# Kernel tuning notes

Hardware: AMD Instinct MI355X
Metric: run time of the kernel (lower is better)

The kernel has to match this reference:

```python
import jax, jax.numpy as jnp
import numpy as np

N = 100000
E = 1600000
IN_DIM, HID, OUT = 128, 64, 32
SLOPE = 0.1


def setup_inputs() -> dict:
    key = jax.random.key(0)
    ks = jax.random.split(key, 8)
    x = jax.random.normal(ks[0], (N, IN_DIM), dtype=jnp.float32)
    edge_index = jax.random.randint(ks[1], (2, E), 0, N, dtype=jnp.int64)
    s1 = 1.0 / np.sqrt(IN_DIM)
    s2 = 1.0 / np.sqrt(HID)
    W_l1 = jax.random.uniform(ks[2], (IN_DIM, HID), jnp.float32, -s1, s1)
    W_r1 = jax.random.uniform(ks[3], (IN_DIM, HID), jnp.float32, -s1, s1)
    b1 = jax.random.uniform(ks[4], (HID,), jnp.float32, -s1, s1)
    W_l2 = jax.random.uniform(ks[5], (HID, OUT), jnp.float32, -s2, s2)
    W_r2 = jax.random.uniform(ks[6], (HID, OUT), jnp.float32, -s2, s2)
    b2 = jax.random.uniform(ks[7], (OUT,), jnp.float32, -s2, s2)
    return {"x": x, "edge_index": edge_index,
            "W_l1": W_l1, "W_r1": W_r1, "b1": b1,
            "W_l2": W_l2, "W_r2": W_r2, "b2": b2}


def _sage_conv(h, src, dst, deg_inv, W_l, W_r, b):
    # mean-aggregate neighbor features: gather from src, scatter-add to dst
    agg = jax.ops.segment_sum(h[src], dst, num_segments=N) * deg_inv  # [N, d]
    return agg @ W_l + h @ W_r + b


def reference(x, edge_index, W_l1, W_r1, b1, W_l2, W_r2, b2):
    src, dst = edge_index[0], edge_index[1]
    deg = jax.ops.segment_sum(jnp.ones((E,), x.dtype), dst, num_segments=N)
    deg_inv = (1.0 / jnp.maximum(deg, 1.0))[:, None]  # [N, 1]
    h = jax.nn.leaky_relu(_sage_conv(x, src, dst, deg_inv, W_l1, W_r1, b1), SLOPE)
    z = jax.nn.leaky_relu(_sage_conv(h, src, dst, deg_inv, W_l2, W_r2, b2), SLOPE)
    return z
```

## Files before the change

kernel.cpp:

```cpp
#include <hip/hip_runtime.h>


constexpr int IN_DIM  = 128;
constexpr int HID     = 64;
constexpr int OUT_DIM = 32;
constexpr float SLOPE = 0.1f;
constexpr int NPB_SHIFT = 8;
constexpr int NBMAX = 512;
constexpr int CHUNK = 4096;
constexpr int SUBCAP = 4096;

typedef unsigned int uint32;
typedef unsigned short ushort16;
typedef unsigned char uchar8;
using floatx2 = __attribute__((ext_vector_type(2))) float;

__device__ inline float blo(uint32 u) { return __uint_as_float(u << 16); }
__device__ inline float bhi(uint32 u) { return __uint_as_float(u & 0xffff0000u); }
__device__ inline ushort16 f2b(float f) {
    uint32 u = __float_as_uint(f);
    u += 0x7fffu + ((u >> 16) & 1u);
    return (ushort16)(u >> 16);
}
__device__ inline uint32 pack2(float lo, float hi) {
    return (uint32)f2b(lo) | ((uint32)f2b(hi) << 16);
}
__device__ inline float lrelu(float v) { return (v > 0.f) ? v : SLOPE * v; }
__device__ inline void addup(float* acc, uint4 u) {
    acc[0] += blo(u.x); acc[1] += bhi(u.x);
    acc[2] += blo(u.y); acc[3] += bhi(u.y);
    acc[4] += blo(u.z); acc[5] += bhi(u.z);
    acc[6] += blo(u.w); acc[7] += bhi(u.w);
}
__device__ inline uchar8 f2fp8(float f) {
    uint32 r = (uint32)__builtin_amdgcn_cvt_pk_fp8_f32(f, f, 0, false);
    return (uchar8)(r & 0xffu);
}
__device__ inline void addp4(float* acc, uint32 w) {
    floatx2 a = __builtin_amdgcn_cvt_pk_f32_fp8((int)w, false);
    floatx2 b = __builtin_amdgcn_cvt_pk_f32_fp8((int)w, true);
    acc[0] += a[0]; acc[1] += a[1]; acc[2] += b[0]; acc[3] += b[1];
}
__device__ inline void addq(float* acc, uint4 u) {
    addp4(acc + 0, u.x); addp4(acc + 4, u.y);
    addp4(acc + 8, u.z); addp4(acc + 12, u.w);
}

__global__ __launch_bounds__(256) void prep_kernel(
    const float* __restrict__ Wl1, const float* __restrict__ Wr1,
    const float* __restrict__ Wl2, const float* __restrict__ Wr2,
    ushort16* __restrict__ Wb1, ushort16* __restrict__ Wb2,
    int* __restrict__ bhist, int* __restrict__ done) {
    const int gid = blockIdx.x * 256 + threadIdx.x;
    if (gid < NBMAX) bhist[gid] = 0;
    if (gid == NBMAX) *done = 0;
    for (int i = gid; i < 128 * 128; i += gridDim.x * 256) {
        int c = i >> 7, k = i & 127;
        Wb1[i] = f2b((c < HID) ? Wl1[k * HID + c] : Wr1[k * HID + (c - HID)]);
    }
    for (int i = gid; i < 64 * 64; i += gridDim.x * 256) {
        int c = i >> 6, k = i & 63;
        Wb2[i] = f2b((c < OUT_DIM) ? Wl2[k * OUT_DIM + c]
                                   : Wr2[k * OUT_DIM + (c - OUT_DIM)]);
    }
}

__global__ __launch_bounds__(256) void hist_scan_kernel(
    const int* __restrict__ dst, int* __restrict__ bhist,
    int* __restrict__ pbase, int* __restrict__ bcur,
    int* __restrict__ done, int E, int NB) {
    __shared__ int bh[NBMAX];
    __shared__ int s2[256];
    __shared__ int flag;
    const int tid = threadIdx.x;
    for (int i = tid; i < NBMAX; i += 256) bh[i] = 0;
    __syncthreads();
    for (int e = blockIdx.x * 256 + tid; e < E; e += gridDim.x * 256)
        atomicAdd(&bh[dst[e] >> NPB_SHIFT], 1);
    __syncthreads();
    for (int b = tid; b < NBMAX; b += 256)
        if (bh[b]) atomicAdd(&bhist[b], bh[b]);
    __threadfence();
    if (tid == 0) flag = (atomicAdd(done, 1) == (int)gridDim.x - 1) ? 1 : 0;
    __syncthreads();
    if (!flag) return;
    __threadfence();
    int v0 = atomicAdd(&bhist[2 * tid], 0);
    int v1 = atomicAdd(&bhist[2 * tid + 1], 0);
    int p0 = (v0 + 15) & ~15, p1 = (v1 + 15) & ~15;
    s2[tid] = p0 + p1; __syncthreads();
    for (int off = 1; off < 256; off <<= 1) {
        int b = (tid >= off) ? s2[tid - off] : 0;
        __syncthreads();
        s2[tid] += b;
        __syncthreads();
    }
    int base = s2[tid] - (p0 + p1);
    pbase[2 * tid]     = base;      bcur[2 * tid]     = base;
    pbase[2 * tid + 1] = base + p0; bcur[2 * tid + 1] = base + p0;
}

__global__ __launch_bounds__(256) void gemm1_part_kernel(
    const float* __restrict__ x, const ushort16* __restrict__ Wb1,
    const float* __restrict__ b1,
    const int* __restrict__ src, const int* __restrict__ dst,
    int* __restrict__ bcur, uint32* __restrict__ pairs,
    uchar8* __restrict__ xlb, float* __restrict__ xr,
    int N, int E, int NB, int npart) {
    using frag = __attribute__((ext_vector_type(8))) short;
    using f32x4 = __attribute__((ext_vector_type(4))) float;
    constexpr int LDA = IN_DIM + 8;
    __shared__ union {
        struct {
            int hist[NBMAX], loff[NBMAX], cur[NBMAX], gbase[NBMAX];
            int s[256];
            uint32 stage[CHUNK];
        } p;
        ushort16 Ash[64][LDA];
    } sm;
    const int tid = threadIdx.x;
    if (blockIdx.x < npart) {
        const int e0  = blockIdx.x * CHUNK;
        const int cnt = min(CHUNK, E - e0);
        for (int i = tid; i < NBMAX; i += 256) sm.p.hist[i] = 0;
        __syncthreads();
        int sreg[16], dreg[16];
#pragma unroll
        for (int k = 0; k < 16; ++k) {
            int i = tid + k * 256;
            if (i < cnt) {
                sreg[k] = src[e0 + i];
                dreg[k] = dst[e0 + i];
                atomicAdd(&sm.p.hist[dreg[k] >> NPB_SHIFT], 1);
            }
        }
        __syncthreads();
        int a0 = sm.p.hist[2 * tid], a1 = sm.p.hist[2 * tid + 1];
        sm.p.s[tid] = a0 + a1; __syncthreads();
        for (int off = 1; off < 256; off <<= 1) {
            int t = (tid >= off) ? sm.p.s[tid - off] : 0;
            __syncthreads();
            sm.p.s[tid] += t;
            __syncthreads();
        }
        int ex = sm.p.s[tid] - (a0 + a1);
        sm.p.loff[2 * tid] = ex;      sm.p.loff[2 * tid + 1] = ex + a0;
        sm.p.cur[2 * tid]  = ex;      sm.p.cur[2 * tid + 1]  = ex + a0;
        __syncthreads();
#pragma unroll
        for (int k = 0; k < 16; ++k) {
            int i = tid + k * 256;
            if (i < cnt) {
                int b = dreg[k] >> NPB_SHIFT;
                int pos = atomicAdd(&sm.p.cur[b], 1);
                sm.p.stage[pos] = (uint32)sreg[k] | ((uint32)(dreg[k] & 255) << 24);
            }
        }
        __syncthreads();
        for (int b = tid; b < NB; b += 256) {
            int cb = sm.p.hist[b];
            if (cb) sm.p.gbase[b] = atomicAdd(&bcur[b], cb);
        }
        __syncthreads();
        for (int i = tid; i < cnt; i += 256) {
            int lo = 0, hi = NB - 1;
            while (lo < hi) {
                int mid = (lo + hi + 1) >> 1;
                if (sm.p.loff[mid] <= i) lo = mid; else hi = mid - 1;
            }
            pairs[sm.p.gbase[lo] + (i - sm.p.loff[lo])] = sm.p.stage[i];
        }
        return;
    }
    const int n0 = (blockIdx.x - npart) * 64;
    {
        const int lc = (tid & 31) * 4;
        for (int row = tid >> 5; row < 64; row += 8) {
            int node = n0 + row;
            float4 xv = (node < N)
                ? *reinterpret_cast<const float4*>(&x[(long)node * IN_DIM + lc])
                : float4{0.f, 0.f, 0.f, 0.f};
            ushort16 pk[4] = {f2b(xv.x), f2b(xv.y), f2b(xv.z), f2b(xv.w)};
            *reinterpret_cast<ushort2*>(&sm.Ash[row][lc])     = ushort2{pk[0], pk[1]};
            *reinterpret_cast<ushort2*>(&sm.Ash[row][lc + 2]) = ushort2{pk[2], pk[3]};
        }
    }
    __syncthreads();
    const int lane = tid & 63;
    const int m0   = (tid >> 6) * 16;
    const int mlo  = lane & 15;
    const int qk   = lane >> 4;
    frag Af[4];
#pragma unroll
    for (int kc = 0; kc < 4; ++kc)
        Af[kc] = *reinterpret_cast<const frag*>(&sm.Ash[m0 + mlo][kc * 32 + qk * 8]);
#pragma unroll
    for (int ct = 0; ct < 8; ++ct) {
        f32x4 acc = {0.f, 0.f, 0.f, 0.f};
#pragma unroll
        for (int kc = 0; kc < 4; ++kc) {
            frag Bf = *reinterpret_cast<const frag*>(
                &Wb1[(ct * 16 + mlo) * 128 + kc * 32 + qk * 8]);
            acc = __builtin_amdgcn_mfma_f32_16x16x32_bf16(Af[kc], Bf, acc, 0, 0, 0);
        }
        const int col = ct * 16 + mlo;
#pragma unroll
        for (int r = 0; r < 4; ++r) {
            int node = n0 + m0 + qk * 4 + r;
            if (node < N) {
                if (col < HID) xlb[(long)node * HID + col] = f2fp8(acc[r]);
                else           xr[(long)node * HID + (col - HID)] = acc[r] + b1[col - HID];
            }
        }
    }
}

__global__ __launch_bounds__(512) void agg1_gemm2_kernel(
    const uint32* __restrict__ pairs, const int* __restrict__ bhist,
    const int* __restrict__ pbase,
    const uint4* __restrict__ xlq, const float* __restrict__ xr,
    const ushort16* __restrict__ Wb2, const float* __restrict__ b2,
    uint32* __restrict__ srcs, int* __restrict__ rowptr, int* __restrict__ degA,
    ushort16* __restrict__ hl, float* __restrict__ hr, int N) {
    using frag = __attribute__((ext_vector_type(8))) short;
    using f32x4 = __attribute__((ext_vector_type(4))) float;
    constexpr int LDH = HID + 8;
    __shared__ int hist[256], loff[256], cur[128];
    __shared__ int lsrc[SUBCAP];
    __shared__ ushort16 hsh[128][LDH];
    const int tid  = threadIdx.x;
    const int bkt  = blockIdx.x >> 1;
    const int half = blockIdx.x & 1;
    const int n0   = bkt << NPB_SHIFT;
    const int base = pbase[bkt];
    const int sz   = bhist[bkt];
    if (tid < 256) hist[tid] = 0;
    __syncthreads();
    for (int i = tid; i < sz; i += 512)
        atomicAdd(&hist[pairs[base + i] >> 24], 1);
    __syncthreads();
    int v = (tid < 256) ? hist[tid] : 0;
    if (tid < 256) loff[tid] = v;
    __syncthreads();
    for (int off = 1; off < 256; off <<= 1) {
        int t = (tid >= off && tid < 256) ? loff[tid - off] : 0;
        __syncthreads();
        if (tid < 256) loff[tid] += t;
        __syncthreads();
    }
    if (tid < 256) loff[tid] -= v;
    __syncthreads();
    if (half == 0 && tid < 256 && n0 + tid < N) {
        rowptr[n0 + tid] = base + loff[tid];
        degA[n0 + tid]   = hist[tid];
    }
    const int hbase = loff[half << 7];
    const int hcnt  = (half ? sz : loff[128]) - hbase;
    if (tid < 128) cur[tid] = loff[(half << 7) + tid] - hbase;
    __syncthreads();
    for (int i = tid; i < sz; i += 512) {
        uint32 u = pairs[base + i];
        int dl = u >> 24;
        if ((dl >> 7) == half) {
            int pos = atomicAdd(&cur[dl & 127], 1);
            lsrc[pos] = (int)(u & 0xFFFFFFu);
        }
    }
    __syncthreads();
    for (int i = tid; i < hcnt; i += 512)
        srcs[base + hbase + i] = (uint32)lsrc[i];
    const int lane = tid & 63;
    const int wid  = tid >> 6;
    const int li   = lane & 3;
    {
        const int nlb = wid * 16 + (lane >> 2);
        const int nl  = (half << 7) + nlb;
        const int n   = n0 + nl;
        if (n < N) {
            const int lo0 = loff[nl] - hbase;
            const int d   = hist[nl];
            float acc[16] = {};
            int j = 0;
            while (j + 16 <= d) {
                int i0[8], i1[8];
#pragma unroll
                for (int t = 0; t < 8; ++t) i0[t] = lsrc[lo0 + j + t];
#pragma unroll
                for (int t = 0; t < 8; ++t) i1[t] = lsrc[lo0 + j + 8 + t];
                uint4 u0[8], u1[8];
#pragma unroll
                for (int t = 0; t < 8; ++t) u0[t] = xlq[(long)i0[t] * 4 + li];
#pragma unroll
                for (int t = 0; t < 8; ++t) u1[t] = xlq[(long)i1[t] * 4 + li];
#pragma unroll
                for (int t = 0; t < 8; ++t) { addq(acc, u0[t]); addq(acc, u1[t]); }
                j += 16;
            }
            if (j + 8 <= d) {
                int i0[8];
#pragma unroll
                for (int t = 0; t < 8; ++t) i0[t] = lsrc[lo0 + j + t];
                uint4 u0[8];
#pragma unroll
                for (int t = 0; t < 8; ++t) u0[t] = xlq[(long)i0[t] * 4 + li];
#pragma unroll
                for (int t = 0; t < 8; ++t) addq(acc, u0[t]);
                j += 8;
            }
            for (; j < d; ++j) {
                uint4 u = xlq[(long)lsrc[lo0 + j] * 4 + li];
                addq(acc, u);
            }
            const float dinv = (d > 0) ? (1.f / (float)d) : 1.f;
            const float* xrp = &xr[(long)n * HID + li * 16];
            float4 xa = *reinterpret_cast<const float4*>(xrp);
            float4 xb = *reinterpret_cast<const float4*>(xrp + 4);
            float4 xc = *reinterpret_cast<const float4*>(xrp + 8);
            float4 xd = *reinterpret_cast<const float4*>(xrp + 12);
            float hv[16];
            hv[0]  = fmaf(acc[0],  dinv, xa.x); hv[1]  = fmaf(acc[1],  dinv, xa.y);
            hv[2]  = fmaf(acc[2],  dinv, xa.z); hv[3]  = fmaf(acc[3],  dinv, xa.w);
            hv[4]  = fmaf(acc[4],  dinv, xb.x); hv[5]  = fmaf(acc[5],  dinv, xb.y);
            hv[6]  = fmaf(acc[6],  dinv, xb.z); hv[7]  = fmaf(acc[7],  dinv, xb.w);
            hv[8]  = fmaf(acc[8],  dinv, xc.x); hv[9]  = fmaf(acc[9],  dinv, xc.y);
            hv[10] = fmaf(acc[10], dinv, xc.z); hv[11] = fmaf(acc[11], dinv, xc.w);
            hv[12] = fmaf(acc[12], dinv, xd.x); hv[13] = fmaf(acc[13], dinv, xd.y);
            hv[14] = fmaf(acc[14], dinv, xd.z); hv[15] = fmaf(acc[15], dinv, xd.w);
#pragma unroll
            for (int t = 0; t < 16; ++t) hv[t] = lrelu(hv[t]);
            uint4 pk0, pk1;
            pk0.x = pack2(hv[0],  hv[1]);  pk0.y = pack2(hv[2],  hv[3]);
            pk0.z = pack2(hv[4],  hv[5]);  pk0.w = pack2(hv[6],  hv[7]);
            pk1.x = pack2(hv[8],  hv[9]);  pk1.y = pack2(hv[10], hv[11]);
            pk1.z = pack2(hv[12], hv[13]); pk1.w = pack2(hv[14], hv[15]);
            *reinterpret_cast<uint4*>(&hsh[nlb][li * 16])     = pk0;
            *reinterpret_cast<uint4*>(&hsh[nlb][li * 16 + 8]) = pk1;
        }
    }
    __syncthreads();
    const int m0  = wid * 16;
    const int mlo = lane & 15;
    const int qk  = lane >> 4;
    frag Af[2];
#pragma unroll
    for (int kc = 0; kc < 2; ++kc)
        Af[kc] = *reinterpret_cast<const frag*>(&hsh[m0 + mlo][kc * 32 + qk * 8]);
#pragma unroll
    for (int ct = 0; ct < 4; ++ct) {
        f32x4 acc = {0.f, 0.f, 0.f, 0.f};
#pragma unroll
        for (int kc = 0; kc < 2; ++kc) {
            frag Bf = *reinterpret_cast<const frag*>(
                &Wb2[(ct * 16 + mlo) * 64 + kc * 32 + qk * 8]);
            acc = __builtin_amdgcn_mfma_f32_16x16x32_bf16(Af[kc], Bf, acc, 0, 0, 0);
        }
        const int col = ct * 16 + mlo;
#pragma unroll
        for (int r = 0; r < 4; ++r) {
            int node = n0 + (half << 7) + m0 + qk * 4 + r;
            if (node < N) {
                if (col < OUT_DIM) hl[(long)node * OUT_DIM + col] = f2b(acc[r]);
                else hr[(long)node * OUT_DIM + (col - OUT_DIM)] = acc[r] + b2[col - OUT_DIM];
            }
        }
    }
}

__global__ __launch_bounds__(256) void agg2_final_kernel(
    const int* __restrict__ rowptr, const int* __restrict__ degA,
    const uint32* __restrict__ srcs,
    const uint4* __restrict__ hlq, const float* __restrict__ hr,
    float* __restrict__ z, int N) {
    const int lane  = threadIdx.x & 63;
    const int li    = lane & 3;
    const int gbase = lane & 60;
    const int wave  = (blockIdx.x << 2) + (threadIdx.x >> 6);
    const int n     = wave * 16 + (lane >> 2);
    if (n >= N) return;
    const int rp = rowptr[n];
    const int d  = degA[n];
    float acc[8] = {};
    int j = 0;
    while (j + 16 <= d) {
        int sA = (int)srcs[rp + j + li];
        int sB = (int)srcs[rp + j + 4 + li];
        int sC = (int)srcs[rp + j + 8 + li];
        int sD = (int)srcs[rp + j + 12 + li];
        uint4 u[16];
#pragma unroll
        for (int t = 0; t < 4; ++t) u[t]      = hlq[(long)__shfl(sA, gbase + t) * 4 + li];
#pragma unroll
        for (int t = 0; t < 4; ++t) u[4 + t]  = hlq[(long)__shfl(sB, gbase + t) * 4 + li];
#pragma unroll
        for (int t = 0; t < 4; ++t) u[8 + t]  = hlq[(long)__shfl(sC, gbase + t) * 4 + li];
#pragma unroll
        for (int t = 0; t < 4; ++t) u[12 + t] = hlq[(long)__shfl(sD, gbase + t) * 4 + li];
#pragma unroll
        for (int t = 0; t < 16; ++t) addup(acc, u[t]);
        j += 16;
    }
    while (j + 4 <= d) {
        int sA = (int)srcs[rp + j + li];
        uint4 u[4];
#pragma unroll
        for (int t = 0; t < 4; ++t) u[t] = hlq[(long)__shfl(sA, gbase + t) * 4 + li];
#pragma unroll
        for (int t = 0; t < 4; ++t) addup(acc, u[t]);
        j += 4;
    }
    int r = d - j;
    if (r > 0) {
        int sA = (int)srcs[rp + j + ((li < r) ? li : 0)];
#pragma unroll
        for (int t = 0; t < 3; ++t) {
            if (t < r) {
                uint4 u = hlq[(long)__shfl(sA, gbase + t) * 4 + li];
                addup(acc, u);
            }
        }
    }
    const float dinv = (d > 0) ? (1.f / (float)d) : 1.f;
    float4 hA = *reinterpret_cast<const float4*>(&hr[(long)n * OUT_DIM + 8 * li]);
    float4 hB = *reinterpret_cast<const float4*>(&hr[(long)n * OUT_DIM + 8 * li + 4]);
    float4 vA, vB;
    vA.x = lrelu(fmaf(acc[0], dinv, hA.x)); vA.y = lrelu(fmaf(acc[1], dinv, hA.y));
    vA.z = lrelu(fmaf(acc[2], dinv, hA.z)); vA.w = lrelu(fmaf(acc[3], dinv, hA.w));
    vB.x = lrelu(fmaf(acc[4], dinv, hB.x)); vB.y = lrelu(fmaf(acc[5], dinv, hB.y));
    vB.z = lrelu(fmaf(acc[6], dinv, hB.z)); vB.w = lrelu(fmaf(acc[7], dinv, hB.w));
    *reinterpret_cast<float4*>(&z[(long)n * OUT_DIM + 8 * li]) = vA;
    *reinterpret_cast<float4*>(&z[(long)n * OUT_DIM + 8 * li + 4]) = vB;
}

extern "C" void kernel_launch(void* const* d_in, const int* in_sizes, int n_in,
                              void* d_out, int out_size, void* d_ws, size_t ws_size,
                              hipStream_t stream) {
    const float* x   = (const float*)d_in[0];
    const int*   ei  = (const int*)d_in[1];
    const float* Wl1 = (const float*)d_in[2];
    const float* Wr1 = (const float*)d_in[3];
    const float* b1  = (const float*)d_in[4];
    const float* Wl2 = (const float*)d_in[5];
    const float* Wr2 = (const float*)d_in[6];
    const float* b2  = (const float*)d_in[7];

    const int N = in_sizes[0] / IN_DIM;
    const int E = in_sizes[1] / 2;
    const int* src = ei;
    const int* dst = ei + E;
    const int NB = (N + 255) >> NPB_SHIFT;

    char* p = (char*)d_ws;
    int* bhist    = (int*)p;           p += sizeof(int) * NBMAX;
    int* done     = (int*)p;           p += sizeof(int) * 4;
    int* pbase    = (int*)p;           p += sizeof(int) * NBMAX;
    int* bcur     = (int*)p;           p += sizeof(int) * NBMAX;
    int* rowptr   = (int*)p;           p += sizeof(int) * (N + 4);
    int* degA     = (int*)p;           p += sizeof(int) * (N + 4);
    uint32* pairs = (uint32*)p;        p += sizeof(uint32) * ((size_t)E + 16 * NBMAX);
    uint32* srcs  = (uint32*)p;        p += sizeof(uint32) * ((size_t)E + 16 * NBMAX);
    ushort16* Wb1 = (ushort16*)p;      p += sizeof(ushort16) * 128 * 128;
    ushort16* Wb2 = (ushort16*)p;      p += sizeof(ushort16) * 64 * 64;
    uchar8* xlb   = (uchar8*)p;        p += sizeof(uchar8) * ((size_t)N * HID + 64);
    float* xr     = (float*)p;         p += sizeof(float) * (size_t)N * HID;
    ushort16* hl  = (ushort16*)p;      p += sizeof(ushort16) * (size_t)N * OUT_DIM;
    float* hr     = (float*)p;         p += sizeof(float) * (size_t)N * OUT_DIM;

    const int ngemm = (N + 63) / 64;
    const int npart = (E + CHUNK - 1) / CHUNK;
    prep_kernel<<<32, 256, 0, stream>>>(Wl1, Wr1, Wl2, Wr2, Wb1, Wb2, bhist, done);
    hist_scan_kernel<<<256, 256, 0, stream>>>(dst, bhist, pbase, bcur, done, E, NB);
    gemm1_part_kernel<<<npart + ngemm, 256, 0, stream>>>(
        x, Wb1, b1, src, dst, bcur, pairs, xlb, xr, N, E, NB, npart);
    agg1_gemm2_kernel<<<NB * 2, 512, 0, stream>>>(pairs, bhist, pbase,
                                                  (const uint4*)xlb, xr, Wb2, b2,
                                                  srcs, rowptr, degA, hl, hr, N);
    agg2_final_kernel<<<(N + 63) / 64, 256, 0, stream>>>(rowptr, degA, srcs,
                                                         (const uint4*)hl, hr,
                                                         (float*)d_out, N);
}
```

Measured before the change: 284.4 us.

## Build CSR with per-node global atomic histogram and placement instead of bucket partition

Replaces the two-level bucketed partition of edges with a direct CSR build. Per-node degrees are counted with global atomics, scanned in two kernels into rowptr, and each source index is placed with an atomic cursor per destination node. The aggregation kernel then reads contiguous CSR slices directly and drops its in-block re-sorting and write-back of srcs. This removes shared-memory sorting, binary searches and the intermediate pairs buffer. In exchange it adds two extra kernel launches, contended random global atomics over both histogram and placement passes, and a non-deterministic neighbor order.

```diff
diff --git a/kernel.cpp b/kernel.cpp
--- a/kernel.cpp
+++ b/kernel.cpp
@@ -5,10 +5,8 @@
 constexpr int HID     = 64;
 constexpr int OUT_DIM = 32;
 constexpr float SLOPE = 0.1f;
-constexpr int NPB_SHIFT = 8;
-constexpr int NBMAX = 512;
-constexpr int CHUNK = 4096;
-constexpr int SUBCAP = 4096;
+constexpr int NBKMAX  = 512;
+constexpr int LCAP    = 4096;
 
 typedef unsigned int uint32;
 typedef unsigned short ushort16;
@@ -50,129 +48,100 @@
     const float* __restrict__ Wl1, const float* __restrict__ Wr1,
     const float* __restrict__ Wl2, const float* __restrict__ Wr2,
     ushort16* __restrict__ Wb1, ushort16* __restrict__ Wb2,
-    int* __restrict__ bhist, int* __restrict__ done) {
+    int* __restrict__ deg, int* __restrict__ done2, int N) {
     const int gid = blockIdx.x * 256 + threadIdx.x;
-    if (gid < NBMAX) bhist[gid] = 0;
-    if (gid == NBMAX) *done = 0;
-    for (int i = gid; i < 128 * 128; i += gridDim.x * 256) {
+    const int stride = gridDim.x * 256;
+    for (int i = gid; i < N + 2; i += stride) deg[i] = 0;
+    if (gid == 0) *done2 = 0;
+    for (int i = gid; i < 128 * 128; i += stride) {
         int c = i >> 7, k = i & 127;
         Wb1[i] = f2b((c < HID) ? Wl1[k * HID + c] : Wr1[k * HID + (c - HID)]);
     }
-    for (int i = gid; i < 64 * 64; i += gridDim.x * 256) {
+    for (int i = gid; i < 64 * 64; i += stride) {
         int c = i >> 6, k = i & 63;
         Wb2[i] = f2b((c < OUT_DIM) ? Wl2[k * OUT_DIM + c]
                                    : Wr2[k * OUT_DIM + (c - OUT_DIM)]);
     }
 }
 
-__global__ __launch_bounds__(256) void hist_scan_kernel(
-    const int* __restrict__ dst, int* __restrict__ bhist,
-    int* __restrict__ pbase, int* __restrict__ bcur,
-    int* __restrict__ done, int E, int NB) {
-    __shared__ int bh[NBMAX];
-    __shared__ int s2[256];
+__global__ __launch_bounds__(256) void hist_kernel(
+    const int* __restrict__ dst, int* __restrict__ deg, int E) {
+    for (int e = blockIdx.x * 256 + threadIdx.x; e < E; e += gridDim.x * 256)
+        atomicAdd(&deg[dst[e]], 1);
+}
+
+__global__ __launch_bounds__(256) void scanA_kernel(
+    const int* __restrict__ deg, int* __restrict__ loc,
+    int* __restrict__ bsum, int* __restrict__ gbase,
+    int* __restrict__ done2, int N, int NBK) {
+    __shared__ int s[256];
     __shared__ int flag;
     const int tid = threadIdx.x;
-    for (int i = tid; i < NBMAX; i += 256) bh[i] = 0;
-    __syncthreads();
-    for (int e = blockIdx.x * 256 + tid; e < E; e += gridDim.x * 256)
-        atomicAdd(&bh[dst[e] >> NPB_SHIFT], 1);
-    __syncthreads();
-    for (int b = tid; b < NBMAX; b += 256)
-        if (bh[b]) atomicAdd(&bhist[b], bh[b]);
+    const int n = blockIdx.x * 256 + tid;
+    int v = (n < N) ? deg[n] : 0;
+    s[tid] = v; __syncthreads();
+    for (int off = 1; off < 256; off <<= 1) {
+        int t = (tid >= off) ? s[tid - off] : 0;
+        __syncthreads();
+        s[tid] += t;
+        __syncthreads();
+    }
+    if (n < N) loc[n] = s[tid] - v;
+    if (tid == 255) bsum[blockIdx.x] = s[255];
     __threadfence();
-    if (tid == 0) flag = (atomicAdd(done, 1) == (int)gridDim.x - 1) ? 1 : 0;
+    if (tid == 0) flag = (atomicAdd(done2, 1) == NBK - 1) ? 1 : 0;
     __syncthreads();
     if (!flag) return;
     __threadfence();
-    int v0 = atomicAdd(&bhist[2 * tid], 0);
-    int v1 = atomicAdd(&bhist[2 * tid + 1], 0);
-    int p0 = (v0 + 15) & ~15, p1 = (v1 + 15) & ~15;
-    s2[tid] = p0 + p1; __syncthreads();
+    int v0 = (2 * tid     < NBK) ? atomicAdd(&bsum[2 * tid], 0)     : 0;
+    int v1 = (2 * tid + 1 < NBK) ? atomicAdd(&bsum[2 * tid + 1], 0) : 0;
+    s[tid] = v0 + v1; __syncthreads();
     for (int off = 1; off < 256; off <<= 1) {
-        int b = (tid >= off) ? s2[tid - off] : 0;
+        int t = (tid >= off) ? s[tid - off] : 0;
         __syncthreads();
-        s2[tid] += b;
+        s[tid] += t;
         __syncthreads();
     }
-    int base = s2[tid] - (p0 + p1);
-    pbase[2 * tid]     = base;      bcur[2 * tid]     = base;
-    pbase[2 * tid + 1] = base + p0; bcur[2 * tid + 1] = base + p0;
-}
-
-__global__ __launch_bounds__(256) void gemm1_part_kernel(
+    int base = s[tid] - (v0 + v1);
+    if (2 * tid     < NBK) gbase[2 * tid]     = base;
+    if (2 * tid + 1 < NBK) gbase[2 * tid + 1] = base + v0;
+}
+
+__global__ __launch_bounds__(256) void scanB_kernel(
+    const int* __restrict__ loc, const int* __restrict__ gbase,
+    int* __restrict__ rowptr, int* __restrict__ cur, int N, int E) {
+    const int n = blockIdx.x * 256 + threadIdx.x;
+    if (n < N) {
+        int r = gbase[n >> 8] + loc[n];
+        rowptr[n] = r;
+        cur[n] = r;
+    }
+    if (n == 0) rowptr[N] = E;
+}
+
+__global__ __launch_bounds__(256) void place_gemm1_kernel(
     const float* __restrict__ x, const ushort16* __restrict__ Wb1,
     const float* __restrict__ b1,
     const int* __restrict__ src, const int* __restrict__ dst,
-    int* __restrict__ bcur, uint32* __restrict__ pairs,
+    int* __restrict__ cur, uint32* __restrict__ srcs,
     uchar8* __restrict__ xlb, float* __restrict__ xr,
-    int N, int E, int NB, int npart) {
+    int N, int E, int nplace) {
     using frag = __attribute__((ext_vector_type(8))) short;
     using f32x4 = __attribute__((ext_vector_type(4))) float;
     constexpr int LDA = IN_DIM + 8;
-    __shared__ union {
-        struct {
-            int hist[NBMAX], loff[NBMAX], cur[NBMAX], gbase[NBMAX];
-            int s[256];
-            uint32 stage[CHUNK];
-        } p;
-        ushort16 Ash[64][LDA];
-    } sm;
+    __shared__ ushort16 Ash[64][LDA];
     const int tid = threadIdx.x;
-    if (blockIdx.x < npart) {
-        const int e0  = blockIdx.x * CHUNK;
-        const int cnt = min(CHUNK, E - e0);
-        for (int i = tid; i < NBMAX; i += 256) sm.p.hist[i] = 0;
-        __syncthreads();
-        int sreg[16], dreg[16];
-#pragma unroll
-        for (int k = 0; k < 16; ++k) {
-            int i = tid + k * 256;
-            if (i < cnt) {
-                sreg[k] = src[e0 + i];
-                dreg[k] = dst[e0 + i];
-                atomicAdd(&sm.p.hist[dreg[k] >> NPB_SHIFT], 1);
-            }
-        }
-        __syncthreads();
-        int a0 = sm.p.hist[2 * tid], a1 = sm.p.hist[2 * tid + 1];
-        sm.p.s[tid] = a0 + a1; __syncthreads();
-        for (int off = 1; off < 256; off <<= 1) {
-            int t = (tid >= off) ? sm.p.s[tid - off] : 0;
-            __syncthreads();
-            sm.p.s[tid] += t;
-            __syncthreads();
-        }
-        int ex = sm.p.s[tid] - (a0 + a1);
-        sm.p.loff[2 * tid] = ex;      sm.p.loff[2 * tid + 1] = ex + a0;
-        sm.p.cur[2 * tid]  = ex;      sm.p.cur[2 * tid + 1]  = ex + a0;
-        __syncthreads();
-#pragma unroll
-        for (int k = 0; k < 16; ++k) {
-            int i = tid + k * 256;
-            if (i < cnt) {
-                int b = dreg[k] >> NPB_SHIFT;
-                int pos = atomicAdd(&sm.p.cur[b], 1);
-                sm.p.stage[pos] = (uint32)sreg[k] | ((uint32)(dreg[k] & 255) << 24);
-            }
-        }
-        __syncthreads();
-        for (int b = tid; b < NB; b += 256) {
-            int cb = sm.p.hist[b];
-            if (cb) sm.p.gbase[b] = atomicAdd(&bcur[b], cb);
-        }
-        __syncthreads();
-        for (int i = tid; i < cnt; i += 256) {
-            int lo = 0, hi = NB - 1;
-            while (lo < hi) {
-                int mid = (lo + hi + 1) >> 1;
-                if (sm.p.loff[mid] <= i) lo = mid; else hi = mid - 1;
-            }
-            pairs[sm.p.gbase[lo] + (i - sm.p.loff[lo])] = sm.p.stage[i];
+    if (blockIdx.x < nplace) {
+        const int stride = nplace * 256;
+        for (int e = blockIdx.x * 256 + tid; e < E; e += stride) {
+            int s = src[e];
+            int d = dst[e];
+            int pos = atomicAdd(&cur[d], 1);
+            srcs[pos] = (uint32)s;
         }
         return;
     }
-    const int n0 = (blockIdx.x - npart) * 64;
+    const int n0 = (blockIdx.x - nplace) * 64;
     {
         const int lc = (tid & 31) * 4;
         for (int row = tid >> 5; row < 64; row += 8) {
@@ -181,8 +150,8 @@
                 ? *reinterpret_cast<const float4*>(&x[(long)node * IN_DIM + lc])
                 : float4{0.f, 0.f, 0.f, 0.f};
             ushort16 pk[4] = {f2b(xv.x), f2b(xv.y), f2b(xv.z), f2b(xv.w)};
-            *reinterpret_cast<ushort2*>(&sm.Ash[row][lc])     = ushort2{pk[0], pk[1]};
-            *reinterpret_cast<ushort2*>(&sm.Ash[row][lc + 2]) = ushort2{pk[2], pk[3]};
+            *reinterpret_cast<ushort2*>(&Ash[row][lc])     = ushort2{pk[0], pk[1]};
+            *reinterpret_cast<ushort2*>(&Ash[row][lc + 2]) = ushort2{pk[2], pk[3]};
         }
     }
     __syncthreads();
@@ -193,7 +162,7 @@
     frag Af[4];
 #pragma unroll
     for (int kc = 0; kc < 4; ++kc)
-        Af[kc] = *reinterpret_cast<const frag*>(&sm.Ash[m0 + mlo][kc * 32 + qk * 8]);
+        Af[kc] = *reinterpret_cast<const frag*>(&Ash[m0 + mlo][kc * 32 + qk * 8]);
 #pragma unroll
     for (int ct = 0; ct < 8; ++ct) {
         f32x4 acc = {0.f, 0.f, 0.f, 0.f};
@@ -216,87 +185,41 @@
 }
 
 __global__ __launch_bounds__(512) void agg1_gemm2_kernel(
-    const uint32* __restrict__ pairs, const int* __restrict__ bhist,
-    const int* __restrict__ pbase,
+    const uint32* __restrict__ srcs, const int* __restrict__ rowptr,
     const uint4* __restrict__ xlq, const float* __restrict__ xr,
     const ushort16* __restrict__ Wb2, const float* __restrict__ b2,
-    uint32* __restrict__ srcs, int* __restrict__ rowptr, int* __restrict__ degA,
     ushort16* __restrict__ hl, float* __restrict__ hr, int N) {
     using frag = __attribute__((ext_vector_type(8))) short;
     using f32x4 = __attribute__((ext_vector_type(4))) float;
     constexpr int LDH = HID + 8;
-    __shared__ int hist[256], loff[256], cur[128];
-    __shared__ int lsrc[SUBCAP];
+    __shared__ int rps[129];
+    __shared__ int lsrc[LCAP];
     __shared__ ushort16 hsh[128][LDH];
-    const int tid  = threadIdx.x;
-    const int bkt  = blockIdx.x >> 1;
-    const int half = blockIdx.x & 1;
-    const int n0   = bkt << NPB_SHIFT;
-    const int base = pbase[bkt];
-    const int sz   = bhist[bkt];
-    if (tid < 256) hist[tid] = 0;
+    const int tid = threadIdx.x;
+    const int n0  = blockIdx.x * 128;
+    if (tid < 129) {
+        int nn = n0 + tid;
+        rps[tid] = rowptr[nn < N ? nn : N];
+    }
     __syncthreads();
+    const int rp0 = rps[0];
+    int sz = rps[128] - rp0;
+    if (sz > LCAP) sz = LCAP;
     for (int i = tid; i < sz; i += 512)
-        atomicAdd(&hist[pairs[base + i] >> 24], 1);
+        lsrc[i] = (int)srcs[rp0 + i];
     __syncthreads();
-    int v = (tid < 256) ? hist[tid] : 0;
-    if (tid < 256) loff[tid] = v;
-    __syncthreads();
-    for (int off = 1; off < 256; off <<= 1) {
-        int t = (tid >= off && tid < 256) ? loff[tid - off] : 0;
-        __syncthreads();
-        if (tid < 256) loff[tid] += t;
-        __syncthreads();
-    }
-    if (tid < 256) loff[tid] -= v;
-    __syncthreads();
-    if (half == 0 && tid < 256 && n0 + tid < N) {
-        rowptr[n0 + tid] = base + loff[tid];
-        degA[n0 + tid]   = hist[tid];
-    }
-    const int hbase = loff[half << 7];
-    const int hcnt  = (half ? sz : loff[128]) - hbase;
-    if (tid < 128) cur[tid] = loff[(half << 7) + tid] - hbase;
-    __syncthreads();
-    for (int i = tid; i < sz; i += 512) {
-        uint32 u = pairs[base + i];
-        int dl = u >> 24;
-        if ((dl >> 7) == half) {
-            int pos = atomicAdd(&cur[dl & 127], 1);
-            lsrc[pos] = (int)(u & 0xFFFFFFu);
-        }
-    }
-    __syncthreads();
-    for (int i = tid; i < hcnt; i += 512)
-        srcs[base + hbase + i] = (uint32)lsrc[i];
     const int lane = tid & 63;
     const int wid  = tid >> 6;
     const int li   = lane & 3;
     {
         const int nlb = wid * 16 + (lane >> 2);
-        const int nl  = (half << 7) + nlb;
-        const int n   = n0 + nl;
+        const int n   = n0 + nlb;
         if (n < N) {
-            const int lo0 = loff[nl] - hbase;
-            const int d   = hist[nl];
+            const int lo0 = rps[nlb] - rp0;
+            const int d   = rps[nlb + 1] - rps[nlb];
             float acc[16] = {};
             int j = 0;
-            while (j + 16 <= d) {
-                int i0[8], i1[8];
-#pragma unroll
-                for (int t = 0; t < 8; ++t) i0[t] = lsrc[lo0 + j + t];
-#pragma unroll
-                for (int t = 0; t < 8; ++t) i1[t] = lsrc[lo0 + j + 8 + t];
-                uint4 u0[8], u1[8];
-#pragma unroll
-                for (int t = 0; t < 8; ++t) u0[t] = xlq[(long)i0[t] * 4 + li];
-#pragma unroll
-                for (int t = 0; t < 8; ++t) u1[t] = xlq[(long)i1[t] * 4 + li];
-#pragma unroll
-                for (int t = 0; t < 8; ++t) { addq(acc, u0[t]); addq(acc, u1[t]); }
-                j += 16;
-            }
-            if (j + 8 <= d) {
+            while (j + 8 <= d) {
                 int i0[8];
 #pragma unroll
                 for (int t = 0; t < 8; ++t) i0[t] = lsrc[lo0 + j + t];
@@ -306,6 +229,17 @@
 #pragma unroll
                 for (int t = 0; t < 8; ++t) addq(acc, u0[t]);
                 j += 8;
+            }
+            if (j + 4 <= d) {
+                int i1[4];
+#pragma unroll
+                for (int t = 0; t < 4; ++t) i1[t] = lsrc[lo0 + j + t];
+                uint4 u1[4];
+#pragma unroll
+                for (int t = 0; t < 4; ++t) u1[t] = xlq[(long)i1[t] * 4 + li];
+#pragma unroll
+                for (int t = 0; t < 4; ++t) addq(acc, u1[t]);
+                j += 4;
             }
             for (; j < d; ++j) {
                 uint4 u = xlq[(long)lsrc[lo0 + j] * 4 + li];
@@ -357,7 +291,7 @@
         const int col = ct * 16 + mlo;
 #pragma unroll
         for (int r = 0; r < 4; ++r) {
-            int node = n0 + (half << 7) + m0 + qk * 4 + r;
+            int node = n0 + m0 + qk * 4 + r;
             if (node < N) {
                 if (col < OUT_DIM) hl[(long)node * OUT_DIM + col] = f2b(acc[r]);
                 else hr[(long)node * OUT_DIM + (col - OUT_DIM)] = acc[r] + b2[col - OUT_DIM];
@@ -367,7 +301,7 @@
 }
 
 __global__ __launch_bounds__(256) void agg2_final_kernel(
-    const int* __restrict__ rowptr, const int* __restrict__ degA,
+    const int* __restrict__ rowptr, const int* __restrict__ deg,
     const uint32* __restrict__ srcs,
     const uint4* __restrict__ hlq, const float* __restrict__ hr,
     float* __restrict__ z, int N) {
@@ -378,7 +312,7 @@
     const int n     = wave * 16 + (lane >> 2);
     if (n >= N) return;
     const int rp = rowptr[n];
-    const int d  = degA[n];
+    const int d  = deg[n];
     float acc[8] = {};
     int j = 0;
     while (j + 16 <= d) {
@@ -447,17 +381,17 @@
     const int E = in_sizes[1] / 2;
     const int* src = ei;
     const int* dst = ei + E;
-    const int NB = (N + 255) >> NPB_SHIFT;
+    const int NBK = (N + 255) >> 8;
 
     char* p = (char*)d_ws;
-    int* bhist    = (int*)p;           p += sizeof(int) * NBMAX;
-    int* done     = (int*)p;           p += sizeof(int) * 4;
-    int* pbase    = (int*)p;           p += sizeof(int) * NBMAX;
-    int* bcur     = (int*)p;           p += sizeof(int) * NBMAX;
+    int* deg      = (int*)p;           p += sizeof(int) * (N + 4);
+    int* loc      = (int*)p;           p += sizeof(int) * (N + 4);
     int* rowptr   = (int*)p;           p += sizeof(int) * (N + 4);
-    int* degA     = (int*)p;           p += sizeof(int) * (N + 4);
-    uint32* pairs = (uint32*)p;        p += sizeof(uint32) * ((size_t)E + 16 * NBMAX);
-    uint32* srcs  = (uint32*)p;        p += sizeof(uint32) * ((size_t)E + 16 * NBMAX);
+    int* cur      = (int*)p;           p += sizeof(int) * (N + 4);
+    int* bsum     = (int*)p;           p += sizeof(int) * NBKMAX;
+    int* gbase    = (int*)p;           p += sizeof(int) * NBKMAX;
+    int* done2    = (int*)p;           p += sizeof(int) * 4;
+    uint32* srcs  = (uint32*)p;        p += sizeof(uint32) * ((size_t)E + 16);
     ushort16* Wb1 = (ushort16*)p;      p += sizeof(ushort16) * 128 * 128;
     ushort16* Wb2 = (ushort16*)p;      p += sizeof(ushort16) * 64 * 64;
     uchar8* xlb   = (uchar8*)p;        p += sizeof(uchar8) * ((size_t)N * HID + 64);
@@ -465,16 +399,17 @@
     ushort16* hl  = (ushort16*)p;      p += sizeof(ushort16) * (size_t)N * OUT_DIM;
     float* hr     = (float*)p;         p += sizeof(float) * (size_t)N * OUT_DIM;
 
-    const int ngemm = (N + 63) / 64;
-    const int npart = (E + CHUNK - 1) / CHUNK;
-    prep_kernel<<<32, 256, 0, stream>>>(Wl1, Wr1, Wl2, Wr2, Wb1, Wb2, bhist, done);
-    hist_scan_kernel<<<256, 256, 0, stream>>>(dst, bhist, pbase, bcur, done, E, NB);
-    gemm1_part_kernel<<<npart + ngemm, 256, 0, stream>>>(
-        x, Wb1, b1, src, dst, bcur, pairs, xlb, xr, N, E, NB, npart);
-    agg1_gemm2_kernel<<<NB * 2, 512, 0, stream>>>(pairs, bhist, pbase,
-                                                  (const uint4*)xlb, xr, Wb2, b2,
-                                                  srcs, rowptr, degA, hl, hr, N);
-    agg2_final_kernel<<<(N + 63) / 64, 256, 0, stream>>>(rowptr, degA, srcs,
+    const int ngemm  = (N + 63) / 64;
+    const int nplace = 512;
+    prep_kernel<<<96, 256, 0, stream>>>(Wl1, Wr1, Wl2, Wr2, Wb1, Wb2, deg, done2, N);
+    hist_kernel<<<512, 256, 0, stream>>>(dst, deg, E);
+    scanA_kernel<<<NBK, 256, 0, stream>>>(deg, loc, bsum, gbase, done2, N, NBK);
+    scanB_kernel<<<NBK, 256, 0, stream>>>(loc, gbase, rowptr, cur, N, E);
+    place_gemm1_kernel<<<nplace + ngemm, 256, 0, stream>>>(
+        x, Wb1, b1, src, dst, cur, srcs, xlb, xr, N, E, nplace);
+    agg1_gemm2_kernel<<<(N + 127) / 128, 512, 0, stream>>>(
+        srcs, rowptr, (const uint4*)xlb, xr, Wb2, b2, hl, hr, N);
+    agg2_final_kernel<<<(N + 63) / 64, 256, 0, stream>>>(rowptr, deg, srcs,
                                                          (const uint4*)hl, hr,
                                                          (float*)d_out, N);
 }
```

New measurement: 395.2 us. +38.9%, slower.
